# Kernel optimization log

Measured on AMD Instinct MI355X. Metric: run time of the kernel, lower is better.

Reference implementation:

```python
import jax, jax.numpy as jnp
import numpy as np

N, D_IN, D_H, N_HEADS, N_CLS = 8192, 384, 64, 4, 6
LN_EPS = 1e-5


def setup_inputs() -> dict:
    key = jax.random.key(0)
    ks = jax.random.split(key, 8)
    x = jax.random.normal(ks[0], (N, D_IN), dtype=jnp.float32)
    proj_w = jax.random.normal(ks[1], (D_IN, D_H), dtype=jnp.float32) / np.sqrt(D_IN)
    proj_b = jnp.zeros((D_H,), jnp.float32)
    head_w = jax.random.normal(ks[2], (N_HEADS, D_H, D_H), dtype=jnp.float32) / np.sqrt(D_H)
    head_b = jnp.zeros((N_HEADS, D_H), jnp.float32)
    attn_w = jnp.ones((N_HEADS,), jnp.float32)  # nn.Parameter(torch.ones(num_heads))
    gamma = jnp.ones((D_H,), jnp.float32)
    beta = jnp.zeros((D_H,), jnp.float32)
    fc_w = jax.random.normal(ks[3], (D_H, N_CLS), dtype=jnp.float32) / np.sqrt(D_H)
    fc_b = jnp.zeros((N_CLS,), jnp.float32)
    return {"x": x, "proj_w": proj_w, "proj_b": proj_b, "head_w": head_w,
            "head_b": head_b, "attn_w": attn_w, "gamma": gamma, "beta": beta,
            "fc_w": fc_w, "fc_b": fc_b}


def _safe_cdist_sq_to_dist(sq):
    # Euclidean distance with zero (sub)gradient at zero distance, matching torch.cdist.
    pos = sq > 0
    return jnp.where(pos, jnp.sqrt(jnp.where(pos, sq, 1.0)), 0.0)


def reference(x, proj_w, proj_b, head_w, head_b, attn_w, gamma, beta, fc_w, fc_b):
    h = jax.nn.relu(x @ proj_w + proj_b)                      # [N, D_H]
    hp = jnp.einsum('nd,hde->hne', h, head_w) + head_b[:, None, :]  # [H, N, D_H]
    sumsq = jnp.sum(hp * hp, axis=-1)                          # [H, N]
    sq = sumsq[:, :, None] + sumsq[:, None, :] - 2.0 * jnp.einsum('hnd,hmd->hnm', hp, hp)
    dist = _safe_cdist_sq_to_dist(jnp.maximum(sq, 0.0))        # [H, N, N]
    scores = jax.nn.softmax(-dist, axis=-1)                    # [H, N, N]
    h_head = jnp.einsum('hnm,hmd->hnd', scores, hp)            # [H, N, D_H]
    aw = jax.nn.softmax(attn_w, axis=0)                        # [H]
    combined = jnp.einsum('h,hnd->nd', aw, h_head)             # [N, D_H]
    mu = jnp.mean(combined, axis=-1, keepdims=True)
    var = jnp.mean((combined - mu) ** 2, axis=-1, keepdims=True)
    normed = (combined - mu) * jax.lax.rsqrt(var + LN_EPS) * gamma + beta
    return normed @ fc_w + fc_b                                # [N, N_CLS]
```

## Files before the change

kernel.cpp:

```cpp
#include <hip/hip_runtime.h>

#define N_TOK 8192
#define D_IN 384
#define D_H 64
#define NHEADS 4
#define NSPLIT 4
#define N_CLS 6
#define LN_EPS 1e-5f

typedef __attribute__((ext_vector_type(8))) short short8;
typedef __attribute__((ext_vector_type(4))) float f32x4;

#define L2E2 2.08136898100560774f

__device__ __forceinline__ unsigned short f2bf(float f) {
    unsigned int u = __float_as_uint(f);
    u += 0x7FFFu + ((u >> 16) & 1u);
    return (unsigned short)(u >> 16);
}
__device__ __forceinline__ float bf2f(unsigned short s) {
    return __uint_as_float(((unsigned int)s) << 16);
}

__device__ __forceinline__ int kperm(int k) {
    return (k & 32) + 2 * (k & 15) + ((k >> 4) & 1);
}

__device__ __forceinline__ void gload_lds16(const void* g, void* l) {
    __builtin_amdgcn_global_load_lds(
        (const __attribute__((address_space(1))) unsigned int*)g,
        (__attribute__((address_space(3))) unsigned int*)l, 16, 0, 0);
}

__global__ __launch_bounds__(512) void stage1_kernel(
    const float* __restrict__ x, const float* __restrict__ proj_w,
    const float* __restrict__ proj_b, const float* __restrict__ head_w,
    const float* __restrict__ head_b,
    unsigned short* __restrict__ hp, unsigned short* __restrict__ Vf,
    float* __restrict__ ssq2)
{
    const int lane = threadIdx.x & 63;
    const int wv   = threadIdx.x >> 6;
    const int rb0  = blockIdx.x * 32;

    __shared__ float h_sh[32][68];
    __shared__ __align__(16) unsigned short vt[NHEADS][4][64][8];

    {
        float acc[4];
        float b = proj_b[lane];
        #pragma unroll
        for (int r = 0; r < 4; ++r) acc[r] = b;
        const float* x0 = x + (size_t)(rb0 + wv * 4) * D_IN;
        #pragma unroll 2
        for (int k4 = 0; k4 < D_IN / 4; ++k4) {
            float w0 = proj_w[(k4 * 4 + 0) * 64 + lane];
            float w1 = proj_w[(k4 * 4 + 1) * 64 + lane];
            float w2 = proj_w[(k4 * 4 + 2) * 64 + lane];
            float w3 = proj_w[(k4 * 4 + 3) * 64 + lane];
            #pragma unroll
            for (int r = 0; r < 4; ++r) {
                float4 xv = *(const float4*)(x0 + r * D_IN + k4 * 4);
                acc[r] = fmaf(xv.x, w0, acc[r]);
                acc[r] = fmaf(xv.y, w1, acc[r]);
                acc[r] = fmaf(xv.z, w2, acc[r]);
                acc[r] = fmaf(xv.w, w3, acc[r]);
            }
        }
        #pragma unroll
        for (int r = 0; r < 4; ++r)
            h_sh[wv * 4 + r][lane] = fmaxf(acc[r], 0.f);
    }
    __syncthreads();

    const int head = wv >> 1;
    const int half = wv & 1;
    float a[16];
    {
        float b = head_b[head * 64 + lane];
        #pragma unroll
        for (int r = 0; r < 16; ++r) a[r] = b;
    }
    const float* wb = head_w + head * 64 * 64;
    #pragma unroll 2
    for (int e4 = 0; e4 < 16; ++e4) {
        float w0 = wb[(e4 * 4 + 0) * 64 + lane];
        float w1 = wb[(e4 * 4 + 1) * 64 + lane];
        float w2 = wb[(e4 * 4 + 2) * 64 + lane];
        float w3 = wb[(e4 * 4 + 3) * 64 + lane];
        #pragma unroll
        for (int r = 0; r < 16; ++r) {
            float4 hv = *(const float4*)&h_sh[half * 16 + r][e4 * 4];
            a[r] = fmaf(hv.x, w0, a[r]);
            a[r] = fmaf(hv.y, w1, a[r]);
            a[r] = fmaf(hv.z, w2, a[r]);
            a[r] = fmaf(hv.w, w3, a[r]);
        }
    }

    #pragma unroll
    for (int r = 0; r < 16; ++r) {
        int kl  = half * 16 + r;
        int row = rb0 + kl;
        unsigned short hb = f2bf(a[r]);
        float hf = bf2f(hb);
        hp[((size_t)head * N_TOK + row) * 64 + lane] = hb;
        int p = kperm(row & 63);
        vt[head][(p >> 3) & 3][lane][p & 7] = hb;
        float s = hf * hf;
        #pragma unroll
        for (int off = 32; off > 0; off >>= 1) s += __shfl_xor(s, off);
        if (lane == 0) ssq2[head * N_TOK + row] = s * L2E2;
    }
    __syncthreads();

    const int kgbase = (rb0 & 32) ? 4 : 0;
    #pragma unroll
    for (int i = 0; i < 2; ++i) {
        int c  = threadIdx.x + 512 * i;
        int hc = c >> 8, rem = c & 255;
        int kg = rem >> 6, d = rem & 63;
        short8 v = *(const short8*)&vt[hc][kg][d][0];
        *(short8*)&Vf[(((size_t)hc * (N_TOK / 8) + (rb0 >> 6) * 8 + kgbase + kg) * 64
                       + d) * 8] = v;
    }
}

__global__ __launch_bounds__(256, 4) void flash_kernel(
    const unsigned short* __restrict__ hp, const unsigned short* __restrict__ Vf,
    const float* __restrict__ ssq2, unsigned short* __restrict__ Og,
    float* __restrict__ Lg)
{
    const int head  = blockIdx.x & 3;
    const int split = blockIdx.x >> 2;
    const int q0    = blockIdx.y * 128;
    const int w     = threadIdx.x >> 6;
    const int lane  = threadIdx.x & 63;
    const int col   = lane & 15;
    const int quad  = lane >> 4;
    const int tid   = threadIdx.x;

    __shared__ __align__(16) unsigned short Psh[4][2][16][64];
    __shared__ __align__(16) unsigned short Kst[4096];
    __shared__ __align__(16) unsigned short Vst[4096];

    const unsigned short* hpH = hp + head * (N_TOK * 64);
    const unsigned short* VfH = Vf + head * (N_TOK * 64);
    const float* ssqH = ssq2 + head * N_TOK;

    const int rb = q0 + w * 32;
    const bool diag_lo = ((rb >> 5) & 1) == 0;

    short8 aQ[2][2];
    float ssqn2[2][4];
    #pragma unroll
    for (int s = 0; s < 2; ++s) {
        const unsigned short* qrow = hpH + (rb + s * 16 + col) * 64;
        aQ[s][0] = *(const short8*)(qrow + quad * 8);
        aQ[s][1] = *(const short8*)(qrow + 32 + quad * 8);
        #pragma unroll
        for (int r = 0; r < 4; ++r)
            ssqn2[s][r] = ssqH[rb + s * 16 + quad * 4 + r];
    }

    const f32x4 zero4 = {0.f, 0.f, 0.f, 0.f};
    f32x4 accO[2][4] = {{zero4, zero4, zero4, zero4}, {zero4, zero4, zero4, zero4}};
    f32x4 accL[2] = {zero4, zero4};
    const short8 ones = {16256,16256,16256,16256,16256,16256,16256,16256};
    const float NEG2L2 = -2.0f * L2E2;

    const int koff0 = (((tid & ~7) | ((tid & 7) ^ ((tid >> 3) & 7))) << 4);
    const int karow = col * 128 + ((quad ^ (col & 7)) << 4);
    const int va    = (quad * 64 + col) << 4;
    const int wcb   = quad * 512 + ((((col >> 2) ^ ((quad & 1) << 2)) << 4))
                      + ((col & 3) << 2);

    const int kt0   = split * 32;
    const int ktend = kt0 + 32;

    {
        const char* kg = (const char*)(hpH + kt0 * 4096);
        gload_lds16(kg + koff0,        (char*)Kst + tid * 16);
        gload_lds16(kg + koff0 + 4096, (char*)Kst + tid * 16 + 4096);
    }
    float smc[4];
    #pragma unroll
    for (int nt = 0; nt < 4; ++nt) smc[nt] = ssqH[kt0 * 64 + nt * 16 + col];
    __syncthreads();

    #pragma unroll 1
    for (int kt = kt0; kt < ktend; ++kt) {
        const bool has_next = (kt + 1 < ktend);

        {
            const char* vg = (const char*)(VfH + kt * 4096);
            gload_lds16(vg + tid * 16,        (char*)Vst + tid * 16);
            gload_lds16(vg + tid * 16 + 4096, (char*)Vst + tid * 16 + 4096);
        }
        float smn[4];
        if (has_next) {
            #pragma unroll
            for (int nt = 0; nt < 4; ++nt)
                smn[nt] = ssqH[(kt + 1) * 64 + nt * 16 + col];
        }

        const char* Kb = (const char*)Kst;

        f32x4 aSA[2][2] = {{zero4, zero4}, {zero4, zero4}};
        {
            short8 k0 = *(const short8*)(Kb + karow);
            short8 k1 = *(const short8*)(Kb + (karow ^ 64));
            short8 k2 = *(const short8*)(Kb + 2048 + karow);
            short8 k3 = *(const short8*)(Kb + 2048 + (karow ^ 64));
            aSA[0][0] = __builtin_amdgcn_mfma_f32_16x16x32_bf16(aQ[0][0], k0, aSA[0][0], 0, 0, 0);
            aSA[0][0] = __builtin_amdgcn_mfma_f32_16x16x32_bf16(aQ[0][1], k1, aSA[0][0], 0, 0, 0);
            aSA[1][0] = __builtin_amdgcn_mfma_f32_16x16x32_bf16(aQ[1][0], k0, aSA[1][0], 0, 0, 0);
            aSA[1][0] = __builtin_amdgcn_mfma_f32_16x16x32_bf16(aQ[1][1], k1, aSA[1][0], 0, 0, 0);
            aSA[0][1] = __builtin_amdgcn_mfma_f32_16x16x32_bf16(aQ[0][0], k2, aSA[0][1], 0, 0, 0);
            aSA[0][1] = __builtin_amdgcn_mfma_f32_16x16x32_bf16(aQ[0][1], k3, aSA[0][1], 0, 0, 0);
            aSA[1][1] = __builtin_amdgcn_mfma_f32_16x16x32_bf16(aQ[1][0], k2, aSA[1][1], 0, 0, 0);
            aSA[1][1] = __builtin_amdgcn_mfma_f32_16x16x32_bf16(aQ[1][1], k3, aSA[1][1], 0, 0, 0);
        }

        #pragma unroll
        for (int s = 0; s < 2; ++s) {
            char* pB = (char*)&Psh[w][s][0][0];
            float pf0[4], pf1[4];
            #pragma unroll
            for (int r = 0; r < 4; ++r) {
                float sq0 = fmaf(aSA[s][0][r], NEG2L2, ssqn2[s][r] + smc[0]);
                pf0[r] = __builtin_amdgcn_exp2f(-__builtin_amdgcn_sqrtf(fmaxf(sq0, 0.f)));
                float sq1 = fmaf(aSA[s][1][r], NEG2L2, ssqn2[s][r] + smc[1]);
                pf1[r] = __builtin_amdgcn_exp2f(-__builtin_amdgcn_sqrtf(fmaxf(sq1, 0.f)));
            }
            #pragma unroll
            for (int r = 0; r < 4; ++r) {
                unsigned int d0 = __builtin_amdgcn_perm(__float_as_uint(pf1[r]),
                                                        __float_as_uint(pf0[r]), 0x07060302u);
                *(unsigned int*)(pB + ((wcb ^ (r << 4)) + r * 128)) = d0;
            }
        }
        if (diag_lo && kt == (rb >> 6) && lane < 16) {
            #pragma unroll
            for (int s = 0; s < 2; ++s) {
                int t = ((rb + s * 16) >> 4) & 3;
                int sc2 = 4 * lane + 2 * (t & 1);
                int ad = lane * 128 + (((lane >> 2) ^ (lane & 7)) << 4) + (sc2 & 15);
                *(unsigned short*)((char*)&Psh[w][s][0][0] + ad) = 0x3F80;
            }
        }

        f32x4 aSB[2][2] = {{zero4, zero4}, {zero4, zero4}};
        {
            short8 k0 = *(const short8*)(Kb + 4096 + karow);
            short8 k1 = *(const short8*)(Kb + 4096 + (karow ^ 64));
            short8 k2 = *(const short8*)(Kb + 6144 + karow);
            short8 k3 = *(const short8*)(Kb + 6144 + (karow ^ 64));
            aSB[0][0] = __builtin_amdgcn_mfma_f32_16x16x32_bf16(aQ[0][0], k0, aSB[0][0], 0, 0, 0);
            aSB[0][0] = __builtin_amdgcn_mfma_f32_16x16x32_bf16(aQ[0][1], k1, aSB[0][0], 0, 0, 0);
            aSB[1][0] = __builtin_amdgcn_mfma_f32_16x16x32_bf16(aQ[1][0], k0, aSB[1][0], 0, 0, 0);
            aSB[1][0] = __builtin_amdgcn_mfma_f32_16x16x32_bf16(aQ[1][1], k1, aSB[1][0], 0, 0, 0);
            aSB[0][1] = __builtin_amdgcn_mfma_f32_16x16x32_bf16(aQ[0][0], k2, aSB[0][1], 0, 0, 0);
            aSB[0][1] = __builtin_amdgcn_mfma_f32_16x16x32_bf16(aQ[0][1], k3, aSB[0][1], 0, 0, 0);
            aSB[1][1] = __builtin_amdgcn_mfma_f32_16x16x32_bf16(aQ[1][0], k2, aSB[1][1], 0, 0, 0);
            aSB[1][1] = __builtin_amdgcn_mfma_f32_16x16x32_bf16(aQ[1][1], k3, aSB[1][1], 0, 0, 0);
        }

        #pragma unroll
        for (int s = 0; s < 2; ++s) {
            char* pB = (char*)&Psh[w][s][0][0];
            float pf2[4], pf3[4];
            #pragma unroll
            for (int r = 0; r < 4; ++r) {
                float sq2 = fmaf(aSB[s][0][r], NEG2L2, ssqn2[s][r] + smc[2]);
                pf2[r] = __builtin_amdgcn_exp2f(-__builtin_amdgcn_sqrtf(fmaxf(sq2, 0.f)));
                float sq3 = fmaf(aSB[s][1][r], NEG2L2, ssqn2[s][r] + smc[3]);
                pf3[r] = __builtin_amdgcn_exp2f(-__builtin_amdgcn_sqrtf(fmaxf(sq3, 0.f)));
            }
            #pragma unroll
            for (int r = 0; r < 4; ++r) {
                unsigned int d1 = __builtin_amdgcn_perm(__float_as_uint(pf3[r]),
                                                        __float_as_uint(pf2[r]), 0x07060302u);
                *(unsigned int*)(pB + (((wcb ^ (r << 4)) + r * 128) ^ 64)) = d1;
            }
        }
        if (!diag_lo && kt == (rb >> 6) && lane < 16) {
            #pragma unroll
            for (int s = 0; s < 2; ++s) {
                int t = ((rb + s * 16) >> 4) & 3;
                int sc2 = 4 * lane + 2 * (t & 1);
                int ad = (lane * 128 + (((lane >> 2) ^ (lane & 7)) << 4) + (sc2 & 15)) ^ 64;
                *(unsigned short*)((char*)&Psh[w][s][0][0] + ad) = 0x3F80;
            }
        }

        __syncthreads();

        if (has_next) {
            const char* kgn = (const char*)(hpH + (kt + 1) * 4096);
            gload_lds16(kgn + koff0,        (char*)Kst + tid * 16);
            gload_lds16(kgn + koff0 + 4096, (char*)Kst + tid * 16 + 4096);
        }

        {
            const char* p0 = (const char*)&Psh[w][0][0][0];
            const char* p1 = (const char*)&Psh[w][1][0][0];
            const char* Vb = (const char*)Vst;
            short8 aP0 = *(const short8*)(p0 + karow);
            short8 aP1 = *(const short8*)(p1 + karow);
            short8 bV[4];
            #pragma unroll
            for (int dt = 0; dt < 4; ++dt)
                bV[dt] = *(const short8*)(Vb + va + dt * 256);
            accL[0] = __builtin_amdgcn_mfma_f32_16x16x32_bf16(aP0, ones, accL[0], 0, 0, 0);
            accL[1] = __builtin_amdgcn_mfma_f32_16x16x32_bf16(aP1, ones, accL[1], 0, 0, 0);
            #pragma unroll
            for (int dt = 0; dt < 4; ++dt) {
                accO[0][dt] = __builtin_amdgcn_mfma_f32_16x16x32_bf16(aP0, bV[dt], accO[0][dt], 0, 0, 0);
                accO[1][dt] = __builtin_amdgcn_mfma_f32_16x16x32_bf16(aP1, bV[dt], accO[1][dt], 0, 0, 0);
            }
            short8 aP0b = *(const short8*)(p0 + (karow ^ 64));
            short8 aP1b = *(const short8*)(p1 + (karow ^ 64));
            #pragma unroll
            for (int dt = 0; dt < 4; ++dt)
                bV[dt] = *(const short8*)(Vb + va + dt * 256 + 4096);
            accL[0] = __builtin_amdgcn_mfma_f32_16x16x32_bf16(aP0b, ones, accL[0], 0, 0, 0);
            accL[1] = __builtin_amdgcn_mfma_f32_16x16x32_bf16(aP1b, ones, accL[1], 0, 0, 0);
            #pragma unroll
            for (int dt = 0; dt < 4; ++dt) {
                accO[0][dt] = __builtin_amdgcn_mfma_f32_16x16x32_bf16(aP0b, bV[dt], accO[0][dt], 0, 0, 0);
                accO[1][dt] = __builtin_amdgcn_mfma_f32_16x16x32_bf16(aP1b, bV[dt], accO[1][dt], 0, 0, 0);
            }
        }

        __syncthreads();
        if (has_next) {
            smc[0] = smn[0]; smc[1] = smn[1]; smc[2] = smn[2]; smc[3] = smn[3];
        }
    }

    unsigned short* og = Og + (size_t)(split * NHEADS + head) * N_TOK * 64;
    float* lg = Lg + (size_t)(split * NHEADS + head) * N_TOK;
    #pragma unroll
    for (int s = 0; s < 2; ++s)
        #pragma unroll
        for (int r = 0; r < 4; ++r) {
            int row = rb + s * 16 + quad * 4 + r;
            #pragma unroll
            for (int dt = 0; dt < 4; ++dt)
                og[row * 64 + dt * 16 + col] = f2bf(accO[s][dt][r]);
            if (col == 0) lg[row] = accL[s][r];
        }
}

__global__ __launch_bounds__(256) void combine_kernel(
    const unsigned short* __restrict__ Og, const float* __restrict__ Lg,
    const float* __restrict__ attn_w, const float* __restrict__ gamma,
    const float* __restrict__ beta, const float* __restrict__ fc_w,
    const float* __restrict__ fc_b, float* __restrict__ out)
{
    const int lane = threadIdx.x & 63;
    const int ty   = threadIdx.x >> 6;
    const int row  = blockIdx.x * 4 + ty;

    float a0 = attn_w[0], a1 = attn_w[1], a2 = attn_w[2], a3 = attn_w[3];
    float m = fmaxf(fmaxf(a0, a1), fmaxf(a2, a3));
    float e0 = __expf(a0 - m), e1 = __expf(a1 - m), e2 = __expf(a2 - m), e3 = __expf(a3 - m);
    float inv = 1.f / (e0 + e1 + e2 + e3);
    float aw[4] = {e0 * inv, e1 * inv, e2 * inv, e3 * inv};

    float c = 0.f;
    #pragma unroll
    for (int hh = 0; hh < NHEADS; ++hh) {
        float l = 0.f, o = 0.f;
        #pragma unroll
        for (int s = 0; s < NSPLIT; ++s) {
            l += Lg[(s * NHEADS + hh) * N_TOK + row];
            o += bf2f(Og[(size_t)((s * NHEADS + hh) * N_TOK + row) * 64 + lane]);
        }
        c += aw[hh] * o * __builtin_amdgcn_rcpf(l);
    }

    float s = c;
    #pragma unroll
    for (int off = 32; off > 0; off >>= 1) s += __shfl_xor(s, off);
    float mu = s * (1.f / 64.f);
    float d = c - mu;
    float v = d * d;
    #pragma unroll
    for (int off = 32; off > 0; off >>= 1) v += __shfl_xor(v, off);
    float normed = d * rsqrtf(v * (1.f / 64.f) + LN_EPS) * gamma[lane] + beta[lane];

    float lg[N_CLS];
    #pragma unroll
    for (int cc = 0; cc < N_CLS; ++cc) {
        float p = normed * fc_w[lane * N_CLS + cc];
        #pragma unroll
        for (int off = 32; off > 0; off >>= 1) p += __shfl_xor(p, off);
        lg[cc] = p;
    }
    if (lane == 0) {
        #pragma unroll
        for (int cc = 0; cc < N_CLS; ++cc)
            out[row * N_CLS + cc] = lg[cc] + fc_b[cc];
    }
}

extern "C" void kernel_launch(void* const* d_in, const int* in_sizes, int n_in,
                              void* d_out, int out_size, void* d_ws, size_t ws_size,
                              hipStream_t stream)
{
    const float* x      = (const float*)d_in[0];
    const float* proj_w = (const float*)d_in[1];
    const float* proj_b = (const float*)d_in[2];
    const float* head_w = (const float*)d_in[3];
    const float* head_b = (const float*)d_in[4];
    const float* attn_w = (const float*)d_in[5];
    const float* gamma  = (const float*)d_in[6];
    const float* beta   = (const float*)d_in[7];
    const float* fc_w   = (const float*)d_in[8];
    const float* fc_b   = (const float*)d_in[9];
    float* out = (float*)d_out;

    char* ws = (char*)d_ws;
    unsigned short* hp = (unsigned short*)(ws);
    unsigned short* Vf = (unsigned short*)(ws + (4u << 20));
    float* ssq2 = (float*)(ws + (8u << 20));
    unsigned short* Og = (unsigned short*)(ws + (8u << 20) + (128u << 10));
    float* Lg   = (float*)(ws + (24u << 20) + (128u << 10));

    stage1_kernel<<<N_TOK / 32, 512, 0, stream>>>(x, proj_w, proj_b, head_w, head_b,
                                                  hp, Vf, ssq2);
    dim3 g2(NHEADS * NSPLIT, N_TOK / 128);
    flash_kernel<<<g2, 256, 0, stream>>>(hp, Vf, ssq2, Og, Lg);
    combine_kernel<<<N_TOK / 4, 256, 0, stream>>>(Og, Lg, attn_w, gamma, beta,
                                                  fc_w, fc_b, out);
}
```

Before: 219.8 us.

## Double-buffer K and V tiles in LDS and drop mid-loop barrier

K and V tiles now live in two-slot LDS buffers. The next tile's K and V are prefetched at the top of each iteration, and the first V tile is loaded in the prologue, so global-to-LDS copies overlap with the QK and PV MFMA work of the current tile. The `__syncthreads` between the P write and the PV stage is removed, since K no longer needs protecting from being overwritten there. This doubles K/V LDS use (about 40KB per block), which tightens occupancy headroom. Correctness now depends on the remaining barriers and wait counts still ordering the async LDS writes against reads of the other slot.

```diff
diff --git a/kernel.cpp b/kernel.cpp
--- a/kernel.cpp
+++ b/kernel.cpp
@@ -141,8 +141,8 @@
     const int tid   = threadIdx.x;
 
     __shared__ __align__(16) unsigned short Psh[4][2][16][64];
-    __shared__ __align__(16) unsigned short Kst[4096];
-    __shared__ __align__(16) unsigned short Vst[4096];
+    __shared__ __align__(16) unsigned short Kst[2][4096];
+    __shared__ __align__(16) unsigned short Vst[2][4096];
 
     const unsigned short* hpH = hp + head * (N_TOK * 64);
     const unsigned short* VfH = Vf + head * (N_TOK * 64);
@@ -180,8 +180,11 @@
 
     {
         const char* kg = (const char*)(hpH + kt0 * 4096);
-        gload_lds16(kg + koff0,        (char*)Kst + tid * 16);
-        gload_lds16(kg + koff0 + 4096, (char*)Kst + tid * 16 + 4096);
+        const char* vg = (const char*)(VfH + kt0 * 4096);
+        gload_lds16(kg + koff0,        (char*)&Kst[0][0] + tid * 16);
+        gload_lds16(kg + koff0 + 4096, (char*)&Kst[0][0] + tid * 16 + 4096);
+        gload_lds16(vg + tid * 16,        (char*)&Vst[0][0] + tid * 16);
+        gload_lds16(vg + tid * 16 + 4096, (char*)&Vst[0][0] + tid * 16 + 4096);
     }
     float smc[4];
     #pragma unroll
@@ -190,21 +193,25 @@
 
     #pragma unroll 1
     for (int kt = kt0; kt < ktend; ++kt) {
+        const int p = (kt - kt0) & 1;
+        const char* Kb = (const char*)&Kst[p][0];
+        const char* Vb = (const char*)&Vst[p][0];
         const bool has_next = (kt + 1 < ktend);
 
-        {
-            const char* vg = (const char*)(VfH + kt * 4096);
-            gload_lds16(vg + tid * 16,        (char*)Vst + tid * 16);
-            gload_lds16(vg + tid * 16 + 4096, (char*)Vst + tid * 16 + 4096);
-        }
         float smn[4];
         if (has_next) {
+            const char* kgn = (const char*)(hpH + (kt + 1) * 4096);
+            const char* vgn = (const char*)(VfH + (kt + 1) * 4096);
+            char* Kn = (char*)&Kst[p ^ 1][0];
+            char* Vn = (char*)&Vst[p ^ 1][0];
+            gload_lds16(kgn + koff0,        Kn + tid * 16);
+            gload_lds16(kgn + koff0 + 4096, Kn + tid * 16 + 4096);
+            gload_lds16(vgn + tid * 16,        Vn + tid * 16);
+            gload_lds16(vgn + tid * 16 + 4096, Vn + tid * 16 + 4096);
             #pragma unroll
             for (int nt = 0; nt < 4; ++nt)
                 smn[nt] = ssqH[(kt + 1) * 64 + nt * 16 + col];
         }
-
-        const char* Kb = (const char*)Kst;
 
         f32x4 aSA[2][2] = {{zero4, zero4}, {zero4, zero4}};
         {
@@ -294,18 +301,9 @@
             }
         }
 
-        __syncthreads();
-
-        if (has_next) {
-            const char* kgn = (const char*)(hpH + (kt + 1) * 4096);
-            gload_lds16(kgn + koff0,        (char*)Kst + tid * 16);
-            gload_lds16(kgn + koff0 + 4096, (char*)Kst + tid * 16 + 4096);
-        }
-
         {
             const char* p0 = (const char*)&Psh[w][0][0][0];
             const char* p1 = (const char*)&Psh[w][1][0][0];
-            const char* Vb = (const char*)Vst;
             short8 aP0 = *(const short8*)(p0 + karow);
             short8 aP1 = *(const short8*)(p1 + karow);
             short8 bV[4];
```

After: 234.0 us. 1.06x slower.
